# Performance work log

Hardware: AMD Instinct MI355X
Metric: run time of the kernel (lower is better)

Reference implementation:

```python
import jax, jax.numpy as jnp
import numpy as np


def conv1x1(x, w, b):
    # 1x1 conv == channel contraction: w [O,I], x [B,I,H,W] -> [B,O,H,W]
    return jnp.einsum('oi,bihw->bohw', w, x) + b[None, :, None, None]


def inorm(x, eps):
    # InstanceNorm2d (no affine): normalize per-sample per-channel over spatial dims
    m = jnp.mean(x, axis=(2, 3), keepdims=True)
    v = jnp.var(x, axis=(2, 3), keepdims=True)
    return (x - m) * jax.lax.rsqrt(v + eps)


def bnorm(x, eps=1e-5):
    # BatchNorm2d in training mode with weight=1, bias=0: batch stats over (B,H,W)
    m = jnp.mean(x, axis=(0, 2, 3), keepdims=True)
    v = jnp.var(x, axis=(0, 2, 3), keepdims=True)
    return (x - m) * jax.lax.rsqrt(v + eps)


def setup_inputs() -> dict:
    key = jax.random.key(0)
    ks = jax.random.split(key, 12)
    B, N, K, Ci, Co = 16, 2000, 9, 256, 128
    s = 0.05
    return {
        'x_row': jax.random.normal(ks[0], (B, Co, N, 1), jnp.float32),
        'x_local': jax.random.normal(ks[1], (B, Ci, N, K), jnp.float32),
        'w_att1': jax.random.normal(ks[2], (Co, Ci), jnp.float32) * s,
        'b_att1': jnp.zeros((Co,), jnp.float32),
        'wq': jax.random.normal(ks[3], (Co, Co), jnp.float32) * s,
        'bq': jnp.zeros((Co,), jnp.float32),
        'wk': jax.random.normal(ks[4], (Co, Co), jnp.float32) * s,
        'bk': jnp.zeros((Co,), jnp.float32),
        'wv': jax.random.normal(ks[5], (Co, Co), jnp.float32) * s,
        'bv': jnp.zeros((Co,), jnp.float32),
        'w_right': jax.random.normal(ks[6], (Co, Ci), jnp.float32) * s,
        'b_right': jnp.zeros((Co,), jnp.float32),
        'w_l1': jax.random.normal(ks[7], (Co, Ci), jnp.float32) * s,
        'b_l1': jnp.zeros((Co,), jnp.float32),
        'w_l2': jax.random.normal(ks[8], (Co, Co), jnp.float32) * s,
        'b_l2': jnp.zeros((Co,), jnp.float32),
        'w_l3': jax.random.normal(ks[9], (Co, Co), jnp.float32) * s,
        'b_l3': jnp.zeros((Co,), jnp.float32),
        'gamma1': jnp.ones((1,), jnp.float32),
    }


def reference(x_row, x_local, w_att1, b_att1, wq, bq, wk, bk, wv, bv,
              w_right, b_right, w_l1, b_l1, w_l2, b_l2, w_l3, b_l3, gamma1):
    # att1: InstanceNorm(eps=1e-3) -> BatchNorm -> ReLU -> 1x1 conv
    xl = conv1x1(jax.nn.relu(bnorm(inorm(x_local, 1e-3))), w_att1, b_att1)
    q = conv1x1(x_row, wq, bq)      # [B,C,N,1]
    k = conv1x1(xl, wk, bk)         # [B,C,N,K]
    v = conv1x1(xl, wv, bv)         # [B,C,N,K]
    att = jax.nn.softmax(q * k, axis=3)             # broadcast q over K
    out_local = jnp.sum(att * v, axis=3, keepdims=True)  # [B,C,N,1]
    h = jnp.concatenate([x_row, out_local], axis=1)      # [B,2C,N,1]
    # ResNet_Block(pre=True): right branch is 1x1 conv shortcut
    x1 = conv1x1(h, w_right, b_right)
    o1 = jax.nn.relu(bnorm(inorm(conv1x1(h, w_l1, b_l1), 1e-5))) + x1
    o2 = jax.nn.relu(bnorm(inorm(conv1x1(o1, w_l2, b_l2), 1e-5))) + o1 + x1
    o3 = jax.nn.relu(bnorm(inorm(conv1x1(o2, w_l3, b_l3), 1e-5)) + x1)
    out = x_row + gamma1 * o3
    return (out + out.mean(axis=1, keepdims=True)) * 0.5
```

## Files before the change

### kernel.cpp

```cpp
#include <hip/hip_runtime.h>
#include <math.h>

#define NB    16
#define CIx   256
#define COx   128
#define NPTS  2000
#define KW    9
#define NKx   18000
#define NTIL  25

typedef short bf16x8 __attribute__((ext_vector_type(8)));
typedef float f32x4  __attribute__((ext_vector_type(4)));

__device__ __forceinline__ ushort f2bf(float f){
  unsigned u = __builtin_bit_cast(unsigned, f);
  u = (u + 0x7fffu + ((u>>16)&1u)) >> 16;
  return (ushort)u;
}
__device__ __forceinline__ float bf2f(ushort h){
  unsigned u = ((unsigned)h)<<16;
  return __builtin_bit_cast(float, u);
}
__device__ __forceinline__ int pi16(int c, int mt){
  return (((c & 3) ^ (mt & 3)) << 2) | (c >> 2);
}

__global__ __launch_bounds__(256) void k_xstats(const float* __restrict__ xl,
    float* __restrict__ sum, float* __restrict__ sumsq){
  int bi = blockIdx.x;
  const float4* p = (const float4*)(xl + (size_t)bi * NKx);
  float s = 0.f, ss = 0.f;
  for (int idx = threadIdx.x; idx < NKx/4; idx += 256){
    float4 v = p[idx];
    s  += v.x + v.y + v.z + v.w;
    ss += v.x*v.x + v.y*v.y + v.z*v.z + v.w*v.w;
  }
  __shared__ float rs[256], rss[256];
  rs[threadIdx.x] = s; rss[threadIdx.x] = ss;
  __syncthreads();
  for (int off = 128; off > 0; off >>= 1){
    if (threadIdx.x < off){ rs[threadIdx.x] += rs[threadIdx.x+off]; rss[threadIdx.x] += rss[threadIdx.x+off]; }
    __syncthreads();
  }
  if (threadIdx.x == 0){ sum[bi] = rs[0]; sumsq[bi] = rss[0]; }
}

__global__ void k_xscale(const float* __restrict__ sum, const float* __restrict__ sumsq,
                         float* __restrict__ mOut, float* __restrict__ sOut){
  int i = threadIdx.x;
  float vl[NB], ml[NB];
  float V = 0.f;
  for (int b = 0; b < NB; b++){
    int bi = b*CIx + i;
    float m = sum[bi] * (1.f/(float)NKx);
    float v = sumsq[bi] * (1.f/(float)NKx) - m*m;
    ml[b] = m; vl[b] = v;
    V += v / (v + 1e-3f);
  }
  V *= (1.f/(float)NB);
  float bs = rsqrtf(V + 1e-5f);
  for (int b = 0; b < NB; b++){
    int bi = b*CIx + i;
    mOut[bi] = ml[b];
    sOut[bi] = rsqrtf(vl[b] + 1e-3f) * bs;
  }
}

__global__ void k_prep_kv(const float* __restrict__ w_att1, const float* __restrict__ wk,
                          const float* __restrict__ wv, const float* __restrict__ b_att1,
                          const float* __restrict__ bk, const float* __restrict__ bv,
                          ushort* __restrict__ Wf, float* __restrict__ bKV){
  int r = blockIdx.x;
  int i = threadIdx.x;
  const float* wr = (r < 128) ? (wk + r*128) : (wv + (r-128)*128);
  float acc = 0.f;
  for (int c = 0; c < 128; c++) acc += wr[c] * w_att1[c*CIx + i];
  Wf[r*256 + i] = f2bf(acc);
  if (i == 0){
    float bacc = (r < 128) ? bk[r] : bv[r-128];
    for (int c = 0; c < 128; c++) bacc += wr[c] * b_att1[c];
    bKV[r] = bacc;
  }
}

__global__ void k_prepW(const float* __restrict__ wq, const float* __restrict__ w_right,
                        const float* __restrict__ w_l1, const float* __restrict__ w_l2,
                        const float* __restrict__ w_l3, const float* __restrict__ b_right,
                        const float* __restrict__ b_l1,
                        ushort* __restrict__ Wq, ushort* __restrict__ W2,
                        ushort* __restrict__ W3, ushort* __restrict__ W4,
                        float* __restrict__ bias2){
  int idx = blockIdx.x*256 + threadIdx.x;
  if (idx < 16384){ Wq[idx] = f2bf(wq[idx]); return; }
  idx -= 16384;
  if (idx < 65536){
    int r = idx >> 8, i = idx & 255;
    W2[idx] = f2bf(r < 128 ? w_right[r*256+i] : w_l1[(r-128)*256+i]);
    return;
  }
  idx -= 65536;
  if (idx < 16384){ W3[idx] = f2bf(w_l2[idx]); return; }
  idx -= 16384;
  if (idx < 16384){ W4[idx] = f2bf(w_l3[idx]); return; }
  idx -= 16384;
  if (idx < 256) bias2[idx] = (idx < 128) ? b_right[idx] : b_l1[idx-128];
}

__global__ __launch_bounds__(256,4) void k_attn_mfma(
    const float* __restrict__ xl,
    const float* __restrict__ mArr, const float* __restrict__ sArr,
    const ushort* __restrict__ Wf, const float* __restrict__ bKV,
    const float* __restrict__ Pq,
    float* __restrict__ out_local)
{
  const int b   = blockIdx.y;
  const int n0  = blockIdx.x * 8;
  const int col0 = n0 * KW;
  const int tid = threadIdx.x;
  const int w   = tid >> 6;
  const int lane = tid & 63;
  const int c16 = lane & 15, g = lane >> 4;

  __shared__ ushort wlds[20480];
  ushort (*elds)[16][72] = (ushort (*)[16][72])wlds;
  float* obuf = (float*)(wlds + 18432);

  f32x4 acc[5][4];
#pragma unroll
  for (int mt = 0; mt < 5; mt++)
#pragma unroll
    for (int j = 0; j < 4; j++) acc[mt][j] = (f32x4)0.f;

  {
    unsigned* fb = (unsigned*)wlds;
#pragma unroll
    for (int zz = 0; zz < 4; zz++){
      int z = tid + 256*zz;
      int io2 = z & 3, cj = 8 + ((z>>2)&7), g_ = (z>>5)&3, s = z>>7;
      fb[((s*5 + 4)*4 + g_)*64 + pi16(cj,4)*4 + io2] = 0u;
    }
  }

  {
    const size_t xb = (size_t)b*CIx*NKx + col0;
    const float* mB = mArr + b*CIx;
    const float* sB = sArr + b*CIx;
#pragma unroll
    for (int kk = 0; kk < 9; kk++){
      int idx = tid + 256*kk;
      int il  = idx / 18;
      int c4  = idx - 18*il;
      int i_l = 2*il;
      int col = 4*c4;
      const float* gp = xl + xb + (size_t)i_l*NKx + col;
      float4 ra = *(const float4*)gp;
      float4 rb = *(const float4*)(gp + NKx);
      float2 mm = *(const float2*)(mB + i_l);
      float2 ssv = *(const float2*)(sB + i_l);
      int s = i_l >> 5, g_ = (i_l >> 3) & 3, io2 = il & 3;
      int mt = c4 >> 2;
      unsigned* dstb = (unsigned*)wlds + ((s*5 + mt)*4 + g_)*64 + io2;
      float a0[4] = {ra.x, ra.y, ra.z, ra.w};
      float a1[4] = {rb.x, rb.y, rb.z, rb.w};
#pragma unroll
      for (int j = 0; j < 4; j++){
        int cj = (col + j) & 15;
        float v0 = fmaxf((a0[j] - mm.x)*ssv.x, 0.f);
        float v1 = fmaxf((a1[j] - mm.y)*ssv.y, 0.f);
        dstb[pi16(cj, mt)*4] = (unsigned)f2bf(v0) | ((unsigned)f2bf(v1) << 16);
      }
    }
  }
  __syncthreads();

  {
    const int ct0 = w, ct1 = w + 4, ct2 = w + 8, ct3 = w + 12;
#pragma unroll
    for (int s = 0; s < 8; s++){
      bf16x8 wf0 = *(const bf16x8*)(Wf + (ct0*16 + c16)*256 + s*32 + g*8);
      bf16x8 wf1 = *(const bf16x8*)(Wf + (ct1*16 + c16)*256 + s*32 + g*8);
      bf16x8 wf2 = *(const bf16x8*)(Wf + (ct2*16 + c16)*256 + s*32 + g*8);
      bf16x8 wf3 = *(const bf16x8*)(Wf + (ct3*16 + c16)*256 + s*32 + g*8);
#pragma unroll
      for (int mt = 0; mt < 5; mt++){
        bf16x8 af = *(const bf16x8*)(wlds + ((s*5 + mt)*4 + g)*128 + pi16(c16, mt)*8);
        acc[mt][0] = __builtin_amdgcn_mfma_f32_16x16x32_bf16(af, wf0, acc[mt][0], 0,0,0);
        acc[mt][1] = __builtin_amdgcn_mfma_f32_16x16x32_bf16(af, wf1, acc[mt][1], 0,0,0);
        acc[mt][2] = __builtin_amdgcn_mfma_f32_16x16x32_bf16(af, wf2, acc[mt][2], 0,0,0);
        acc[mt][3] = __builtin_amdgcn_mfma_f32_16x16x32_bf16(af, wf3, acc[mt][3], 0,0,0);
      }
    }
  }
  __syncthreads();

  const int chA = w*16 + c16;
  float2 qa, qb;
  {
    const float* p0 = Pq + ((size_t)(b*COx + chA))*NPTS + n0 + 2*g;
    qa = *(const float2*)p0;
    qb = *(const float2*)(p0 + 64*NPTS);
  }
  float bk0 = bKV[chA], bk1 = bKV[chA + 64];
  float bv0 = bKV[128 + chA], bv1 = bKV[128 + chA + 64];

#pragma unroll
  for (int mt = 0; mt < 5; mt++){
    if (mt < 4 || g < 2){
      int colb = 16*mt + 4*g;
#pragma unroll
      for (int j = 0; j < 4; j++){
#pragma unroll
        for (int r2 = 0; r2 < 2; r2++){
          unsigned pk = (unsigned)f2bf(acc[mt][j][2*r2]) | ((unsigned)f2bf(acc[mt][j][2*r2+1]) << 16);
          *(unsigned*)&elds[w*4 + j][c16][colb + 2*r2] = pk;
        }
      }
    }
  }
  __syncthreads();

#pragma unroll
  for (int h = 0; h < 2; h++){
    float bk_ = h ? bk1 : bk0;
    float bv_ = h ? bv1 : bv0;
    int ch = chA + 64*h;
    const ushort* eK = &elds[w*4 + h][c16][0];
    const ushort* eV = &elds[w*4 + 2 + h][c16][0];
#pragma unroll
    for (int t = 0; t < 2; t++){
      int nloc = 2*g + t;
      int cb = 9*nloc;
      float qq = h ? (t ? qb.y : qb.x) : (t ? qa.y : qa.x);
      float sc[KW];
      float mx = -1e30f;
#pragma unroll
      for (int k = 0; k < KW; k++){
        float s_ = qq * (bf2f(eK[cb + k]) + bk_);
        sc[k] = s_;
        mx = fmaxf(mx, s_);
      }
      float den = 0.f, num = 0.f;
#pragma unroll
      for (int k = 0; k < KW; k++){
        float e = __expf(sc[k] - mx);
        den += e;
        num += e * (bf2f(eV[cb + k]) + bv_);
      }
      obuf[ch*8 + nloc] = num / den;
    }
  }
  __syncthreads();

  {
    int ch = tid >> 1, part = tid & 1;
    float4 v = *(float4*)&obuf[ch*8 + 4*part];
    *(float4*)(out_local + ((size_t)(b*COx + ch))*NPTS + n0 + 4*part) = v;
  }
}

template<int MODE>
__global__ __launch_bounds__(256) void k_mconv(
    const float* __restrict__ inA, const float* __restrict__ inB,
    const ushort* __restrict__ Wc, const float* __restrict__ bias,
    const float* __restrict__ nm, const float* __restrict__ nsc,
    float* __restrict__ out0, float* __restrict__ out1,
    float* __restrict__ uout, float* __restrict__ pstat)
{
  constexpr int IC = (MODE==1) ? 256 : 128;
  constexpr int RC = (MODE==1) ? 256 : 128;
  constexpr int NS = IC/32;
  constexpr int JW = RC/64;
  constexpr int PHASES = RC/128;
  constexpr bool STATS = (MODE >= 1);
  constexpr int SPH = (MODE==1) ? 1 : 0;

  const int b = blockIdx.y, bx = blockIdx.x;
  const int n0 = bx*80;
  const int tid = threadIdx.x;
  const int w = tid>>6, lane = tid&63;
  const int c16 = lane&15, g = lane>>4;

  __shared__ ushort smem[21504];

  {
    constexpr int TOT = (IC/2)*20;
    const float* srcA = inA + (size_t)b*128*NPTS;
    const float* srcB = inB ? (inB + (size_t)b*128*NPTS) : nullptr;
    for (int idx = tid; idx < TOT; idx += 256){
      int pr = idx/20, c4 = idx - 20*pr;
      int i = pr*2;
      int cc = n0 + 4*c4;
      float4 va, vb;
      if (MODE == 0){
        const float* base = srcA + (size_t)i*NPTS + cc;
        va = *(const float4*)base;
        vb = *(const float4*)(base + NPTS);
      } else if (MODE == 1){
        const float* base = (i < 128) ? (srcA + (size_t)i*NPTS + cc)
                                      : (srcB + (size_t)(i-128)*NPTS + cc);
        va = *(const float4*)base;
        vb = *(const float4*)(base + NPTS);
      } else {
        const float* pa = srcA + (size_t)i*NPTS + cc;
        const float* pb = srcB + (size_t)i*NPTS + cc;
        float4 ca = *(const float4*)pa, cb = *(const float4*)(pa+NPTS);
        float4 aa = *(const float4*)pb, ab = *(const float4*)(pb+NPTS);
        float m0 = nm[b*128+i],   s0 = nsc[b*128+i];
        float m1 = nm[b*128+i+1], s1 = nsc[b*128+i+1];
        va.x = fmaxf((ca.x-m0)*s0,0.f)+aa.x; va.y = fmaxf((ca.y-m0)*s0,0.f)+aa.y;
        va.z = fmaxf((ca.z-m0)*s0,0.f)+aa.z; va.w = fmaxf((ca.w-m0)*s0,0.f)+aa.w;
        vb.x = fmaxf((cb.x-m1)*s1,0.f)+ab.x; vb.y = fmaxf((cb.y-m1)*s1,0.f)+ab.y;
        vb.z = fmaxf((cb.z-m1)*s1,0.f)+ab.z; vb.w = fmaxf((cb.w-m1)*s1,0.f)+ab.w;
        if (MODE == 2){
          float4 u0, u1;
          u0.x = va.x+aa.x; u0.y = va.y+aa.y; u0.z = va.z+aa.z; u0.w = va.w+aa.w;
          u1.x = vb.x+ab.x; u1.y = vb.y+ab.y; u1.z = vb.z+ab.z; u1.w = vb.w+ab.w;
          *(float4*)(uout + ((size_t)(b*128+i))*NPTS + cc) = u0;
          *(float4*)(uout + ((size_t)(b*128+i+1))*NPTS + cc) = u1;
        }
      }
      int sp = i>>5, g_ = (i>>3)&3, io2 = (i>>1)&3;
      int mt = c4>>2;
      unsigned* dstb = (unsigned*)smem + ((sp*5 + mt)*4 + g_)*64 + io2;
      float a0[4] = {va.x, va.y, va.z, va.w};
      float a1[4] = {vb.x, vb.y, vb.z, vb.w};
#pragma unroll
      for (int j = 0; j < 4; j++){
        int cj = (4*c4 + j) & 15;
        int pi = pi16(cj, mt);
        dstb[pi*4] = (unsigned)f2bf(a0[j]) | ((unsigned)f2bf(a1[j]) << 16);
      }
    }
  }
  __syncthreads();

  f32x4 acc[5][JW];
#pragma unroll
  for (int mt = 0; mt < 5; mt++)
#pragma unroll
    for (int j = 0; j < JW; j++) acc[mt][j] = (f32x4)0.f;

  for (int s = 0; s < NS; s++){
    bf16x8 wf[JW];
#pragma unroll
    for (int j = 0; j < JW; j++)
      wf[j] = *(const bf16x8*)(Wc + ((w + 4*j)*16 + c16)*IC + s*32 + g*8);
#pragma unroll
    for (int mt = 0; mt < 5; mt++){
      bf16x8 af = *(const bf16x8*)(smem + ((s*5 + mt)*4 + g)*128 + pi16(c16, mt)*8);
#pragma unroll
      for (int j = 0; j < JW; j++)
        acc[mt][j] = __builtin_amdgcn_mfma_f32_16x16x32_bf16(af, wf[j], acc[mt][j], 0,0,0);
    }
  }

  float* dl = (float*)smem;
#pragma unroll
  for (int ph = 0; ph < PHASES; ph++){
    __syncthreads();
    float st_s[2], st_ss[2];
#pragma unroll
    for (int jj = 0; jj < 2; jj++){
      int j = ph*2 + jj;
      int ct = w + 4*j;
      int rl = (ct & 7)*16 + c16;
      float bb = bias[ct*16 + c16];
      float s = 0.f, ss = 0.f;
#pragma unroll
      for (int mt = 0; mt < 5; mt++){
        f32x4 v = acc[mt][j];
        float4 vv;
        vv.x = v[0]+bb; vv.y = v[1]+bb; vv.z = v[2]+bb; vv.w = v[3]+bb;
        *(float4*)&dl[rl*84 + mt*16 + 4*g] = vv;
        s  += vv.x + vv.y + vv.z + vv.w;
        ss += vv.x*vv.x + vv.y*vv.y + vv.z*vv.z + vv.w*vv.w;
      }
      st_s[jj] = s; st_ss[jj] = ss;
    }
    if (STATS && ph == SPH){
#pragma unroll
      for (int jj = 0; jj < 2; jj++){
        float s = st_s[jj], ss = st_ss[jj];
        s += __shfl_xor(s, 16); ss += __shfl_xor(ss, 16);
        s += __shfl_xor(s, 32); ss += __shfl_xor(ss, 32);
        if (g == 0){
          int ct = w + 4*(ph*2 + jj);
          int rl = (ct & 7)*16 + c16;
          size_t pb = (((size_t)b*NTIL + bx)*128 + rl)*2;
          pstat[pb]   = s;
          pstat[pb+1] = ss;
        }
      }
    }
    __syncthreads();
    float* dst = ph ? out1 : out0;
#pragma unroll
    for (int kk = 0; kk < 10; kk++){
      int idx = kk*256 + tid;
      int r = idx/20, c4 = idx - 20*r;
      *(float4*)(dst + ((size_t)(b*128 + r))*NPTS + n0 + 4*c4) = *(float4*)&dl[r*84 + 4*c4];
    }
  }
}

__global__ void k_red(const float* __restrict__ pstat, float* __restrict__ cm, float* __restrict__ cs){
  int c = threadIdx.x;
  float ml[NB], vl[NB];
  float V = 0.f;
  for (int b = 0; b < NB; b++){
    float s = 0.f, ss = 0.f;
    for (int t = 0; t < NTIL; t++){
      size_t base = (((size_t)b*NTIL + t)*128 + c)*2;
      s  += pstat[base];
      ss += pstat[base+1];
    }
    float m = s * (1.f/(float)NPTS);
    float v = ss * (1.f/(float)NPTS) - m*m;
    ml[b] = m; vl[b] = v;
    V += v / (v + 1e-5f);
  }
  V *= (1.f/(float)NB);
  float bs = rsqrtf(V + 1e-5f);
  for (int b = 0; b < NB; b++){
    cm[b*COx + c] = ml[b];
    cs[b*COx + c] = rsqrtf(vl[b] + 1e-5f) * bs;
  }
}

__global__ __launch_bounds__(256) void k_final(const float* __restrict__ c3, const float* __restrict__ x1,
    const float* __restrict__ x_row, const float* __restrict__ cm, const float* __restrict__ cs,
    const float* __restrict__ gamma1, float* __restrict__ out)
{
  const int b  = blockIdx.y;
  const int n0 = blockIdx.x * 50;
  const int tid = threadIdx.x;
  const float g = gamma1[0];
  __shared__ float tt[128][50];
  __shared__ float part[4][50];
  for (int idx = tid; idx < 128*50; idx += 256){
    int c = idx / 50; int j = idx - c*50;
    size_t off = ((size_t)b*COx + c)*NPTS + n0 + j;
    float o3 = fmaxf((c3[off] - cm[b*COx + c]) * cs[b*COx + c] + x1[off], 0.f);
    tt[c][j] = x_row[off] + g * o3;
  }
  __syncthreads();
  if (tid < 200){
    int gg = tid / 50, j = tid - gg*50;
    float s = 0.f;
    for (int c = gg*32; c < gg*32 + 32; c++) s += tt[c][j];
    part[gg][j] = s;
  }
  __syncthreads();
  for (int idx = tid; idx < 128*50; idx += 256){
    int c = idx / 50; int j = idx - c*50;
    float mean = (part[0][j] + part[1][j] + part[2][j] + part[3][j]) * (1.f/128.f);
    out[((size_t)b*COx + c)*NPTS + n0 + j] = 0.5f * (tt[c][j] + mean);
  }
}

extern "C" void kernel_launch(void* const* d_in, const int* in_sizes, int n_in,
                              void* d_out, int out_size, void* d_ws, size_t ws_size,
                              hipStream_t stream){
  (void)in_sizes; (void)n_in; (void)out_size; (void)ws_size;
  const float* x_row   = (const float*)d_in[0];
  const float* x_local = (const float*)d_in[1];
  const float* w_att1  = (const float*)d_in[2];
  const float* b_att1  = (const float*)d_in[3];
  const float* wq      = (const float*)d_in[4];
  const float* bq      = (const float*)d_in[5];
  const float* wk      = (const float*)d_in[6];
  const float* bk      = (const float*)d_in[7];
  const float* wv      = (const float*)d_in[8];
  const float* bv      = (const float*)d_in[9];
  const float* w_right = (const float*)d_in[10];
  const float* b_right = (const float*)d_in[11];
  const float* w_l1    = (const float*)d_in[12];
  const float* b_l1    = (const float*)d_in[13];
  const float* w_l2    = (const float*)d_in[14];
  const float* b_l2    = (const float*)d_in[15];
  const float* w_l3    = (const float*)d_in[16];
  const float* b_l3    = (const float*)d_in[17];
  const float* gamma1  = (const float*)d_in[18];
  float* out = (float*)d_out;

  float*  ws     = (float*)d_ws;
  float*  sum    = ws;
  float*  sumsq  = ws + 4096;
  float*  mArr   = ws + 8192;
  float*  sArr   = ws + 12288;
  ushort* Wf     = (ushort*)(ws + 16384);
  float*  bKV    = ws + 49152;
  ushort* Wq     = (ushort*)(ws + 49408);
  ushort* W2     = (ushort*)(ws + 57600);
  ushort* W3     = (ushort*)(ws + 90368);
  ushort* W4     = (ushort*)(ws + 98560);
  float*  bias2  = ws + 106752;
  float*  cm     = ws + 107008;
  float*  cs     = ws + 109056;
  float*  pstat  = ws + 111104;
  float*  P0 = ws + 262144;
  float*  P1 = P0 + 4096000;
  float*  P2 = P1 + 4096000;
  float*  P3 = P2 + 4096000;

  k_xstats <<<4096, 256, 0, stream>>>(x_local, sum, sumsq);
  k_xscale <<<1, 256, 0, stream>>>(sum, sumsq, mArr, sArr);
  k_prep_kv<<<256, 256, 0, stream>>>(w_att1, wk, wv, b_att1, bk, bv, Wf, bKV);
  k_prepW  <<<450, 256, 0, stream>>>(wq, w_right, w_l1, w_l2, w_l3, b_right, b_l1,
                                     Wq, W2, W3, W4, bias2);

  k_mconv<0><<<dim3(NTIL, NB), 256, 0, stream>>>(x_row, nullptr, Wq, bq,
                                                 nullptr, nullptr, P1, nullptr, nullptr, nullptr);

  k_attn_mfma<<<dim3(250, NB), 256, 0, stream>>>(x_local, mArr, sArr, Wf, bKV, P1, P0);

  k_mconv<1><<<dim3(NTIL, NB), 256, 0, stream>>>(x_row, P0, W2, bias2,
                                                 nullptr, nullptr, P1, P2, nullptr, pstat);
  k_red<<<1, 128, 0, stream>>>(pstat, cm, cs);

  k_mconv<2><<<dim3(NTIL, NB), 256, 0, stream>>>(P2, P1, W3, b_l2,
                                                 cm, cs, P3, nullptr, P0, pstat);
  k_red<<<1, 128, 0, stream>>>(pstat, cm, cs);

  k_mconv<3><<<dim3(NTIL, NB), 256, 0, stream>>>(P3, P0, W4, b_l3,
                                                 cm, cs, P2, nullptr, nullptr, pstat);
  k_red<<<1, 128, 0, stream>>>(pstat, cm, cs);

  k_final<<<dim3(NPTS/50, NB), 256, 0, stream>>>(P2, P1, x_row, cm, cs, gamma1, out);
}
```

Measured before the change: 365.0 us.

## Pre-normalize x_local to bf16 MFMA layout and parallelize stat reduction

Adds a separate kernel that normalizes x_local, converts it to bf16 and stores it in the exact LDS fragment layout the attention kernel expects. The attention kernel then copies it straight into LDS with global_load_lds instead of doing the fp32 loads, normalization and swizzled scatter itself. The stats reduction is also spread over 1024 threads with a split sum/sumsq layout. This adds a full extra pass over x_local (fp32 read plus bf16 write and re-read), trading extra total traffic for a cheaper attention-kernel prologue. The attention kernel's occupancy hint also drops from 4 to 3.

```diff
diff --git a/kernel.cpp b/kernel.cpp
--- a/kernel.cpp
+++ b/kernel.cpp
@@ -8,9 +8,12 @@
 #define KW    9
 #define NKx   18000
 #define NTIL  25
+#define NWND  250
+#define PSTRIDE 51200
 
 typedef short bf16x8 __attribute__((ext_vector_type(8)));
 typedef float f32x4  __attribute__((ext_vector_type(4)));
+typedef unsigned short us8 __attribute__((ext_vector_type(8)));
 
 __device__ __forceinline__ ushort f2bf(float f){
   unsigned u = __builtin_bit_cast(unsigned, f);
@@ -63,6 +66,46 @@
     int bi = b*CIx + i;
     mOut[bi] = ml[b];
     sOut[bi] = rsqrtf(vl[b] + 1e-3f) * bs;
+  }
+}
+
+__global__ __launch_bounds__(256) void k_xnorm(
+    const float* __restrict__ xl, const float* __restrict__ mArr, const float* __restrict__ sArr,
+    ushort* __restrict__ xlb)
+{
+  const int b = blockIdx.y, wnd = blockIdx.x;
+  const int tid = threadIdx.x;
+  __shared__ ushort T[80*264];
+  for (int z = tid; z < 8*264; z += 256) T[72*264 + z] = 0;
+  const int col0 = wnd*72;
+  const float* mB = mArr + b*CIx;
+  const float* sB = sArr + b*CIx;
+#pragma unroll
+  for (int it = 0; it < 18; it++){
+    int idx = it*256 + tid;
+    int i  = idx / 18;
+    int c4 = idx - 18*i;
+    const float* gp = xl + (size_t)(b*CIx + i)*NKx + col0 + 4*c4;
+    float4 v = *(const float4*)gp;
+    float m = mB[i], s = sB[i];
+    float a[4] = {v.x, v.y, v.z, v.w};
+#pragma unroll
+    for (int j = 0; j < 4; j++){
+      float t = fmaxf((a[j] - m)*s, 0.f);
+      T[(4*c4 + j)*264 + i] = f2bf(t);
+    }
+  }
+  __syncthreads();
+  ushort* outp = xlb + ((size_t)b*NWND + wnd)*20480;
+#pragma unroll
+  for (int it = 0; it < 10; it++){
+    int v8 = it*256 + tid;
+    int k = v8 >> 6;
+    int l = v8 & 63;
+    int s = k/5, mt = k - 5*s;
+    int g = l >> 4, c16 = l & 15;
+    us8 val = *(const us8*)&T[(mt*16 + c16)*264 + s*32 + g*8];
+    *(us8*)(outp + (size_t)v8*8) = val;
   }
 }
 
@@ -106,16 +149,14 @@
   if (idx < 256) bias2[idx] = (idx < 128) ? b_right[idx] : b_l1[idx-128];
 }
 
-__global__ __launch_bounds__(256,4) void k_attn_mfma(
-    const float* __restrict__ xl,
-    const float* __restrict__ mArr, const float* __restrict__ sArr,
+__global__ __launch_bounds__(256,3) void k_attn_mfma(
+    const ushort* __restrict__ xlb,
     const ushort* __restrict__ Wf, const float* __restrict__ bKV,
     const float* __restrict__ Pq,
     float* __restrict__ out_local)
 {
   const int b   = blockIdx.y;
   const int n0  = blockIdx.x * 8;
-  const int col0 = n0 * KW;
   const int tid = threadIdx.x;
   const int w   = tid >> 6;
   const int lane = tid & 63;
@@ -125,53 +166,23 @@
   ushort (*elds)[16][72] = (ushort (*)[16][72])wlds;
   float* obuf = (float*)(wlds + 18432);
 
+  {
+    const ushort* src = xlb + ((size_t)b*NWND + blockIdx.x)*20480;
+#pragma unroll
+    for (int j = 0; j < 10; j++){
+      int k = w*10 + j;
+      const unsigned int* gp = (const unsigned int*)(const void*)(src + (size_t)k*512 + lane*8);
+      unsigned int* lp = (unsigned int*)(void*)(&wlds[k*512]);
+      __builtin_amdgcn_global_load_lds(gp, lp, 16, 0, 0);
+    }
+  }
+  __syncthreads();
+
   f32x4 acc[5][4];
 #pragma unroll
   for (int mt = 0; mt < 5; mt++)
 #pragma unroll
     for (int j = 0; j < 4; j++) acc[mt][j] = (f32x4)0.f;
-
-  {
-    unsigned* fb = (unsigned*)wlds;
-#pragma unroll
-    for (int zz = 0; zz < 4; zz++){
-      int z = tid + 256*zz;
-      int io2 = z & 3, cj = 8 + ((z>>2)&7), g_ = (z>>5)&3, s = z>>7;
-      fb[((s*5 + 4)*4 + g_)*64 + pi16(cj,4)*4 + io2] = 0u;
-    }
-  }
-
-  {
-    const size_t xb = (size_t)b*CIx*NKx + col0;
-    const float* mB = mArr + b*CIx;
-    const float* sB = sArr + b*CIx;
-#pragma unroll
-    for (int kk = 0; kk < 9; kk++){
-      int idx = tid + 256*kk;
-      int il  = idx / 18;
-      int c4  = idx - 18*il;
-      int i_l = 2*il;
-      int col = 4*c4;
-      const float* gp = xl + xb + (size_t)i_l*NKx + col;
-      float4 ra = *(const float4*)gp;
-      float4 rb = *(const float4*)(gp + NKx);
-      float2 mm = *(const float2*)(mB + i_l);
-      float2 ssv = *(const float2*)(sB + i_l);
-      int s = i_l >> 5, g_ = (i_l >> 3) & 3, io2 = il & 3;
-      int mt = c4 >> 2;
-      unsigned* dstb = (unsigned*)wlds + ((s*5 + mt)*4 + g_)*64 + io2;
-      float a0[4] = {ra.x, ra.y, ra.z, ra.w};
-      float a1[4] = {rb.x, rb.y, rb.z, rb.w};
-#pragma unroll
-      for (int j = 0; j < 4; j++){
-        int cj = (col + j) & 15;
-        float v0 = fmaxf((a0[j] - mm.x)*ssv.x, 0.f);
-        float v1 = fmaxf((a1[j] - mm.y)*ssv.y, 0.f);
-        dstb[pi16(cj, mt)*4] = (unsigned)f2bf(v0) | ((unsigned)f2bf(v1) << 16);
-      }
-    }
-  }
-  __syncthreads();
 
   {
     const int ct0 = w, ct1 = w + 4, ct2 = w + 8, ct3 = w + 12;
@@ -183,7 +194,7 @@
       bf16x8 wf3 = *(const bf16x8*)(Wf + (ct3*16 + c16)*256 + s*32 + g*8);
 #pragma unroll
       for (int mt = 0; mt < 5; mt++){
-        bf16x8 af = *(const bf16x8*)(wlds + ((s*5 + mt)*4 + g)*128 + pi16(c16, mt)*8);
+        bf16x8 af = *(const bf16x8*)(wlds + ((s*5 + mt)*4 + g)*128 + c16*8);
         acc[mt][0] = __builtin_amdgcn_mfma_f32_16x16x32_bf16(af, wf0, acc[mt][0], 0,0,0);
         acc[mt][1] = __builtin_amdgcn_mfma_f32_16x16x32_bf16(af, wf1, acc[mt][1], 0,0,0);
         acc[mt][2] = __builtin_amdgcn_mfma_f32_16x16x32_bf16(af, wf2, acc[mt][2], 0,0,0);
@@ -386,9 +397,9 @@
         if (g == 0){
           int ct = w + 4*(ph*2 + jj);
           int rl = (ct & 7)*16 + c16;
-          size_t pb = (((size_t)b*NTIL + bx)*128 + rl)*2;
-          pstat[pb]   = s;
-          pstat[pb+1] = ss;
+          int off = (b*NTIL + bx)*128 + rl;
+          pstat[off]           = s;
+          pstat[PSTRIDE + off] = ss;
         }
       }
     }
@@ -403,27 +414,33 @@
   }
 }
 
-__global__ void k_red(const float* __restrict__ pstat, float* __restrict__ cm, float* __restrict__ cs){
-  int c = threadIdx.x;
-  float ml[NB], vl[NB];
-  float V = 0.f;
-  for (int b = 0; b < NB; b++){
+__global__ __launch_bounds__(1024) void k_red(const float* __restrict__ pstat,
+                                              float* __restrict__ cm, float* __restrict__ cs){
+  __shared__ float msh[2048], vsh[2048], wsh[2048];
+  int t = threadIdx.x;
+#pragma unroll
+  for (int h = 0; h < 2; h++){
+    int p = t + h*1024;
+    int b = p >> 7, c = p & 127;
     float s = 0.f, ss = 0.f;
-    for (int t = 0; t < NTIL; t++){
-      size_t base = (((size_t)b*NTIL + t)*128 + c)*2;
-      s  += pstat[base];
-      ss += pstat[base+1];
+    for (int tt = 0; tt < NTIL; tt++){
+      int off = (b*NTIL + tt)*128 + c;
+      s  += pstat[off];
+      ss += pstat[PSTRIDE + off];
     }
     float m = s * (1.f/(float)NPTS);
     float v = ss * (1.f/(float)NPTS) - m*m;
-    ml[b] = m; vl[b] = v;
-    V += v / (v + 1e-5f);
-  }
-  V *= (1.f/(float)NB);
-  float bs = rsqrtf(V + 1e-5f);
-  for (int b = 0; b < NB; b++){
-    cm[b*COx + c] = ml[b];
-    cs[b*COx + c] = rsqrtf(vl[b] + 1e-5f) * bs;
+    msh[p] = m; vsh[p] = v; wsh[p] = v/(v + 1e-5f);
+  }
+  __syncthreads();
+  if (t < 128){
+    float V = 0.f;
+    for (int b = 0; b < NB; b++) V += wsh[b*128 + t];
+    float bs = rsqrtf(V*(1.f/(float)NB) + 1e-5f);
+    for (int b = 0; b < NB; b++){
+      cm[b*COx + t] = msh[b*128 + t];
+      cs[b*COx + t] = rsqrtf(vsh[b*128 + t] + 1e-5f) * bs;
+    }
   }
 }
 
@@ -502,6 +519,7 @@
   float*  P1 = P0 + 4096000;
   float*  P2 = P1 + 4096000;
   float*  P3 = P2 + 4096000;
+  ushort* xlb = (ushort*)(P3 + 4096000);
 
   k_xstats <<<4096, 256, 0, stream>>>(x_local, sum, sumsq);
   k_xscale <<<1, 256, 0, stream>>>(sum, sumsq, mArr, sArr);
@@ -509,22 +527,24 @@
   k_prepW  <<<450, 256, 0, stream>>>(wq, w_right, w_l1, w_l2, w_l3, b_right, b_l1,
                                      Wq, W2, W3, W4, bias2);
 
+  k_xnorm<<<dim3(NWND, NB), 256, 0, stream>>>(x_local, mArr, sArr, xlb);
+
   k_mconv<0><<<dim3(NTIL, NB), 256, 0, stream>>>(x_row, nullptr, Wq, bq,
                                                  nullptr, nullptr, P1, nullptr, nullptr, nullptr);
 
-  k_attn_mfma<<<dim3(250, NB), 256, 0, stream>>>(x_local, mArr, sArr, Wf, bKV, P1, P0);
+  k_attn_mfma<<<dim3(NWND, NB), 256, 0, stream>>>(xlb, Wf, bKV, P1, P0);
 
   k_mconv<1><<<dim3(NTIL, NB), 256, 0, stream>>>(x_row, P0, W2, bias2,
                                                  nullptr, nullptr, P1, P2, nullptr, pstat);
-  k_red<<<1, 128, 0, stream>>>(pstat, cm, cs);
+  k_red<<<1, 1024, 0, stream>>>(pstat, cm, cs);
 
   k_mconv<2><<<dim3(NTIL, NB), 256, 0, stream>>>(P2, P1, W3, b_l2,
                                                  cm, cs, P3, nullptr, P0, pstat);
-  k_red<<<1, 128, 0, stream>>>(pstat, cm, cs);
+  k_red<<<1, 1024, 0, stream>>>(pstat, cm, cs);
 
   k_mconv<3><<<dim3(NTIL, NB), 256, 0, stream>>>(P3, P0, W4, b_l3,
                                                  cm, cs, P2, nullptr, nullptr, pstat);
-  k_red<<<1, 128, 0, stream>>>(pstat, cm, cs);
+  k_red<<<1, 1024, 0, stream>>>(pstat, cm, cs);
 
   k_final<<<dim3(NPTS/50, NB), 256, 0, stream>>>(P2, P1, x_row, cm, cs, gamma1, out);
 }
```

Result: no change. 367.3 us (+0.6%).
